# Kernel tuning notes

Hardware: AMD Instinct MI355X
Metric: run time of the kernel (lower is better)

## Reference

```python
import jax, jax.numpy as jnp
import numpy as np


def _silu(v):
    return v * jax.nn.sigmoid(v)


def setup_inputs() -> dict:
    key = jax.random.key(0)
    ks = jax.random.split(key, 12)
    B, N, DS = 4, 12500, 63      # batch, nodes per graph, dim_single
    E = 800000                   # total edges (avg degree 16)
    BN = B * N
    ND = DS + 1                  # node_dim = dim_single + 1 (timestep channel)
    H, ED = 128, 32              # hidden_dim, edge_dim (fixed in __init__)
    MIN = 2 * ND + ED            # m_input feature dim = 160

    def lin(k, i, o):
        return (jax.random.normal(k, (i, o)) / np.sqrt(i)).astype(jnp.float32)

    return {
        "x": jax.random.normal(ks[0], (B, N, 3), dtype=jnp.float32) * 5.0,
        "cond": jax.random.normal(ks[1], (B, N, DS), dtype=jnp.float32),
        "edge_dist": jax.random.uniform(ks[2], (E,), dtype=jnp.float32) * 15.0,
        "ew1": lin(ks[3], 1, ED), "eb1": jnp.zeros((ED,), jnp.float32),
        "ew2": lin(ks[4], ED, ED), "eb2": jnp.zeros((ED,), jnp.float32),
        "nw1": lin(ks[5], MIN, H), "nb1": jnp.zeros((H,), jnp.float32),
        "nw2": lin(ks[6], H, ND), "nb2": jnp.zeros((ND,), jnp.float32),
        "cw1": lin(ks[7], MIN, H), "cb1": jnp.zeros((H,), jnp.float32),
        "cw2": lin(ks[8], H, 1),
        "edge_index": jax.random.randint(ks[9], (2, E), 0, BN, dtype=jnp.int64 if jax.config.jax_enable_x64 else jnp.int32),
        "t": 100,
    }


def reference(x, cond, edge_dist, ew1, eb1, ew2, eb2, nw1, nb1, nw2, nb2,
              cw1, cb1, cw2, edge_index, t):
    B, N, _ = x.shape
    BN = B * N
    # append timestep scalar channel to conditioning -> node features h
    t_feat = jnp.full((B, N, 1), t, dtype=x.dtype)
    h = jnp.concatenate([cond, t_feat], axis=-1).reshape(BN, -1)   # [BN, node_dim]
    xf = x.reshape(BN, 3)

    src, dst = edge_index[0], edge_index[1]
    # edge_mlp on scalar distances -> [E, edge_dim]
    edge_attr = _silu(edge_dist[:, None] @ ew1 + eb1) @ ew2 + eb2
    # gather + concat -> [E, 2*node_dim + edge_dim]
    m_input = jnp.concatenate([h[src], h[dst], edge_attr], axis=-1)
    # node_mlp (its output h_agg is discarded by p_sample, kept for faithfulness)
    m = _silu(m_input @ nw1 + nb1) @ nw2 + nb2
    h_agg = jax.ops.segment_sum(m, dst, num_segments=BN)
    h_out = h + h_agg  # unused by p_sample's return
    del h_out
    # coord_mlp -> scalar weight per edge
    coord_weight = _silu(m_input @ cw1 + cb1) @ cw2                 # [E, 1]
    dir_vec = xf[src] - xf[dst]                                     # [E, 3]
    dir_len = jnp.maximum(jnp.linalg.norm(dir_vec, axis=-1, keepdims=True), 1e-8)
    coord_update = coord_weight * (dir_vec / dir_len)
    x_agg = jax.ops.segment_sum(coord_update, dst, num_segments=BN)
    return (xf + x_agg).reshape(B, N, 3)
```

## Files before the change

### kernel.cpp

```cpp
#include <hip/hip_runtime.h>
#include <hip/hip_bf16.h>

typedef __attribute__((ext_vector_type(8))) short bf16x8;
typedef __attribute__((ext_vector_type(4))) float f32x4;
typedef __attribute__((ext_vector_type(4), aligned(4))) float f32x4u;
typedef __attribute__((ext_vector_type(2), aligned(4))) float f32x2u;

__device__ __forceinline__ unsigned short f2bf(float f) {
    unsigned int u = __float_as_uint(f);
    unsigned int r = (u + 0x7fffu + ((u >> 16) & 1u)) >> 16;
    return (unsigned short)r;
}
__device__ __forceinline__ float bf2f(unsigned short u) {
    return __uint_as_float(((unsigned int)u) << 16);
}

__global__ void init_out_kernel(const float* __restrict__ x, float* __restrict__ out, int n) {
    int i = blockIdx.x * blockDim.x + threadIdx.x;
    if (i < n) out[i] = x[i];
}

__global__ void prep_bt2_kernel(const float* __restrict__ cw1, unsigned short* __restrict__ bt2) {
    int idx = blockIdx.x * 256 + threadIdx.x;
    if (idx < 256 * 64) {
        int n = idx >> 6, k = idx & 63;
        float v = 0.f;
        if (k < 63) v = (n < 128) ? cw1[k * 128 + n] : cw1[(64 + k) * 128 + (n - 128)];
        bt2[n * 64 + k] = f2bf(v);
    }
}

__global__ void prep_consts_kernel(const float* __restrict__ ew2, const float* __restrict__ eb2,
                                   const float* __restrict__ cw1, const float* __restrict__ cb1,
                                   const int* __restrict__ tptr,
                                   unsigned short* __restrict__ bt_M, float* __restrict__ c0) {
    int j = threadIdx.x;
    float t = (float)tptr[0];
    float cacc = cb1[j] + t * (cw1[63 * 128 + j] + cw1[127 * 128 + j]);
    float m[32];
    #pragma unroll
    for (int p = 0; p < 32; ++p) m[p] = 0.f;
    for (int i = 0; i < 32; ++i) {
        float w = cw1[(128 + i) * 128 + j];
        cacc = fmaf(eb2[i], w, cacc);
        #pragma unroll
        for (int p = 0; p < 32; ++p) m[p] = fmaf(ew2[p * 32 + i], w, m[p]);
    }
    c0[j] = cacc;
    #pragma unroll
    for (int p = 0; p < 32; ++p) bt_M[j * 32 + p] = f2bf(m[p]);
}

__device__ __forceinline__ bf16x8 load8_bf(const float* p) {
    f32x4u a = *(const f32x4u*)p;
    f32x4u b = *(const f32x4u*)(p + 4);
    bf16x8 r;
    r[0] = f2bf(a[0]); r[1] = f2bf(a[1]); r[2] = f2bf(a[2]); r[3] = f2bf(a[3]);
    r[4] = f2bf(b[0]); r[5] = f2bf(b[1]); r[6] = f2bf(b[2]); r[7] = f2bf(b[3]);
    return r;
}
__device__ __forceinline__ bf16x8 load7z_bf(const float* p) {
    f32x4u a = *(const f32x4u*)p;
    f32x2u b = *(const f32x2u*)(p + 4);
    float c = p[6];
    bf16x8 r;
    r[0] = f2bf(a[0]); r[1] = f2bf(a[1]); r[2] = f2bf(a[2]); r[3] = f2bf(a[3]);
    r[4] = f2bf(b[0]); r[5] = f2bf(b[1]); r[6] = f2bf(c);  r[7] = 0;
    return r;
}

__global__ __launch_bounds__(256) void prep_uv_kernel(
    const float* __restrict__ cond, const unsigned short* __restrict__ bt2,
    unsigned short* __restrict__ UV, int BN)
{
    const int tid = threadIdx.x, lane = tid & 63, wid = tid >> 6;
    const int fr = lane & 15, kq = lane >> 4;
    int node = blockIdx.x * 64 + wid * 16 + fr;
    if (node >= BN) node = BN - 1;

    const float* cp = cond + (long)node * 63;
    bf16x8 b0 = load8_bf(cp + 8 * kq);
    bf16x8 b1 = (kq < 3) ? load8_bf(cp + 32 + 8 * kq) : load7z_bf(cp + 56);

    char* UVb = (char*)UV;
    const unsigned off = ((unsigned)node * 256u + (unsigned)(kq * 4)) * 2u;

    #pragma unroll
    for (int n = 0; n < 16; ++n) {
        bf16x8 a0 = *reinterpret_cast<const bf16x8*>(&bt2[(n * 16 + fr) * 64 + 8 * kq]);
        bf16x8 a1 = *reinterpret_cast<const bf16x8*>(&bt2[(n * 16 + fr) * 64 + 32 + 8 * kq]);
        f32x4 acc = (f32x4){0.f, 0.f, 0.f, 0.f};
        acc = __builtin_amdgcn_mfma_f32_16x16x32_bf16(a0, b0, acc, 0, 0, 0);
        acc = __builtin_amdgcn_mfma_f32_16x16x32_bf16(a1, b1, acc, 0, 0, 0);
        uint2 pk;
        pk.x = (unsigned)f2bf(acc[0]) | ((unsigned)f2bf(acc[1]) << 16);
        pk.y = (unsigned)f2bf(acc[2]) | ((unsigned)f2bf(acc[3]) << 16);
        *reinterpret_cast<uint2*>(UVb + off + n * 32) = pk;
    }
}

__global__ __launch_bounds__(256, 4) void edge_kernel(
    const float* __restrict__ x, const float* __restrict__ edge_dist,
    const float* __restrict__ ew1, const float* __restrict__ eb1,
    const unsigned short* __restrict__ bt_M, const float* __restrict__ c0f,
    const float* __restrict__ cw2, const unsigned short* __restrict__ UV,
    const int* __restrict__ edge_index, float* __restrict__ out, int E)
{
    __shared__ __align__(16) unsigned short s_lds[128][40];
    __shared__ int srcl[128];
    __shared__ int dstl[128];
    __shared__ float cw_lds[128];

    const int tid = threadIdx.x, lane = tid & 63, wid = tid >> 6;
    const int fr = lane & 15, kq = lane >> 4;
    const int e0 = blockIdx.x * 128;

    {
        int ei = e0 + (tid & 127); if (ei >= E) ei = E - 1;
        if (tid < 128) srcl[tid] = edge_index[ei];
        else           dstl[tid - 128] = edge_index[E + ei];

        int eh = tid >> 1;
        int e  = e0 + eh; if (e >= E) e = E - 1;
        int j0 = (tid & 1) * 16;
        float dist = edge_dist[e];
        #pragma unroll
        for (int i = 0; i < 8; ++i) {
            float v0 = fmaf(dist, ew1[j0 + 2 * i],     eb1[j0 + 2 * i]);
            float v1 = fmaf(dist, ew1[j0 + 2 * i + 1], eb1[j0 + 2 * i + 1]);
            float s0 = v0 / (1.f + __expf(-v0));
            float s1 = v1 / (1.f + __expf(-v1));
            unsigned pk = (unsigned)f2bf(s0) | ((unsigned)f2bf(s1) << 16);
            *reinterpret_cast<unsigned*>(&s_lds[eh][j0 + 2 * i]) = pk;
        }
    }
    __syncthreads();

    bf16x8 a[2];
    #pragma unroll
    for (int m = 0; m < 2; ++m)
        a[m] = *reinterpret_cast<const bf16x8*>(&s_lds[wid * 32 + m * 16 + fr][8 * kq]);

    unsigned bu[2][4], bv[2][4];
    #pragma unroll
    for (int m = 0; m < 2; ++m)
        #pragma unroll
        for (int r = 0; r < 4; ++r) {
            int row = wid * 32 + m * 16 + kq * 4 + r;
            bu[m][r] = ((unsigned)srcl[row] * 256u + (unsigned)fr) * 2u;
            bv[m][r] = ((unsigned)dstl[row] * 256u + 128u + (unsigned)fr) * 2u;
        }

    const char* UVb = (const char*)UV;
    float psum[2][4] = {{0.f,0.f,0.f,0.f},{0.f,0.f,0.f,0.f}};

    #pragma unroll 1
    for (int nh = 0; nh < 2; ++nh) {
        f32x4 acc[2][4];
        #pragma unroll
        for (int n = 0; n < 4; ++n) {
            float c = c0f[(nh * 4 + n) * 16 + fr];
            acc[0][n] = (f32x4){c, c, c, c};
            acc[1][n] = (f32x4){c, c, c, c};
        }
        #pragma unroll
        for (int n = 0; n < 4; ++n) {
            int col = (nh * 4 + n) * 16 + fr;
            bf16x8 b = *reinterpret_cast<const bf16x8*>(&bt_M[col * 32 + 8 * kq]);
            acc[0][n] = __builtin_amdgcn_mfma_f32_16x16x32_bf16(a[0], b, acc[0][n], 0, 0, 0);
            acc[1][n] = __builtin_amdgcn_mfma_f32_16x16x32_bf16(a[1], b, acc[1][n], 0, 0, 0);
        }
        #pragma unroll
        for (int n = 0; n < 4; ++n) {
            float w2 = cw2[(nh * 4 + n) * 16 + fr];
            const int cb = (nh * 4 + n) * 32;
            #pragma unroll
            for (int m = 0; m < 2; ++m)
                #pragma unroll
                for (int r = 0; r < 4; ++r) {
                    unsigned short uu = *reinterpret_cast<const unsigned short*>(UVb + bu[m][r] + cb);
                    unsigned short vv = *reinterpret_cast<const unsigned short*>(UVb + bv[m][r] + cb);
                    float h = acc[m][n][r] + bf2f(uu) + bf2f(vv);
                    float sil = h / (1.f + __expf(-h));
                    psum[m][r] = fmaf(sil, w2, psum[m][r]);
                }
        }
    }

    #pragma unroll
    for (int off = 1; off < 16; off <<= 1)
        #pragma unroll
        for (int m = 0; m < 2; ++m)
            #pragma unroll
            for (int r = 0; r < 4; ++r)
                psum[m][r] += __shfl_xor(psum[m][r], off, 64);
    if (fr == 0) {
        #pragma unroll
        for (int m = 0; m < 2; ++m) {
            int row0 = wid * 32 + m * 16 + kq * 4;
            #pragma unroll
            for (int r = 0; r < 4; ++r) cw_lds[row0 + r] = psum[m][r];
        }
    }
    __syncthreads();

    if (tid < 128) {
        int e = e0 + tid;
        if (e < E) {
            float coord_w = cw_lds[tid];
            int src = srcl[tid];
            int dst = dstl[tid];
            float dx = x[src * 3 + 0] - x[dst * 3 + 0];
            float dy = x[src * 3 + 1] - x[dst * 3 + 1];
            float dz = x[src * 3 + 2] - x[dst * 3 + 2];
            float len = sqrtf(fmaf(dx, dx, fmaf(dy, dy, dz * dz)));
            len = fmaxf(len, 1e-8f);
            float sc = coord_w / len;
            atomicAdd(&out[dst * 3 + 0], sc * dx);
            atomicAdd(&out[dst * 3 + 1], sc * dy);
            atomicAdd(&out[dst * 3 + 2], sc * dz);
        }
    }
}

extern "C" void kernel_launch(void* const* d_in, const int* in_sizes, int n_in,
                              void* d_out, int out_size, void* d_ws, size_t ws_size,
                              hipStream_t stream) {
    const float* x         = (const float*)d_in[0];
    const float* cond      = (const float*)d_in[1];
    const float* edge_dist = (const float*)d_in[2];
    const float* ew1       = (const float*)d_in[3];
    const float* eb1       = (const float*)d_in[4];
    const float* ew2       = (const float*)d_in[5];
    const float* eb2       = (const float*)d_in[6];
    const float* cw1       = (const float*)d_in[11];
    const float* cb1       = (const float*)d_in[12];
    const float* cw2       = (const float*)d_in[13];
    const int*   edge_index= (const int*)d_in[14];
    const int*   tptr      = (const int*)d_in[15];
    float* out = (float*)d_out;

    const int E  = in_sizes[2];
    const int BN = in_sizes[1] / 63;
    const int n_out = out_size;

    char* ws = (char*)d_ws;
    unsigned short* bt_M = (unsigned short*)(ws);
    float*          c0   = (float*)(ws + 8192);
    unsigned short* bt2  = (unsigned short*)(ws + 16384);
    unsigned short* UV   = (unsigned short*)(ws + 65536);

    init_out_kernel<<<(n_out + 255) / 256, 256, 0, stream>>>(x, out, n_out);
    prep_bt2_kernel<<<64, 256, 0, stream>>>(cw1, bt2);
    prep_consts_kernel<<<1, 128, 0, stream>>>(ew2, eb2, cw1, cb1, tptr, bt_M, c0);
    prep_uv_kernel<<<(BN + 63) / 64, 256, 0, stream>>>(cond, bt2, UV, BN);

    int blocks = (E + 127) / 128;
    edge_kernel<<<blocks, 256, 0, stream>>>(x, edge_dist, ew1, eb1,
                                            bt_M, c0, cw2, UV,
                                            edge_index, out, E);
}
```

Baseline: 307.7 us.

## Transpose MFMA operands so each lane gathers contiguous bf16 hidden features per edge

Swaps the MFMA operand roles so the weight matrix is the A operand and edge features the B operand. Each lane then owns one edge and four consecutive hidden columns. The per-node U/V gathers become one 8-byte load of four packed bf16 values instead of four scalar 2-byte loads at scattered rows. The final reduction shrinks from a 4-step 16-lane shuffle tree on eight values to two shuffles on two values. Edge-MLP setup is also reassigned: half the threads compute the edge features and the other half load indices. This may unbalance that setup phase.

```diff
diff --git a/kernel.cpp b/kernel.cpp
--- a/kernel.cpp
+++ b/kernel.cpp
@@ -11,9 +11,8 @@
     unsigned int r = (u + 0x7fffu + ((u >> 16) & 1u)) >> 16;
     return (unsigned short)r;
 }
-__device__ __forceinline__ float bf2f(unsigned short u) {
-    return __uint_as_float(((unsigned int)u) << 16);
-}
+__device__ __forceinline__ float bflo(unsigned int u) { return __uint_as_float(u << 16); }
+__device__ __forceinline__ float bfhi(unsigned int u) { return __uint_as_float(u & 0xffff0000u); }
 
 __global__ void init_out_kernel(const float* __restrict__ x, float* __restrict__ out, int n) {
     int i = blockIdx.x * blockDim.x + threadIdx.x;
@@ -115,92 +114,86 @@
     const int fr = lane & 15, kq = lane >> 4;
     const int e0 = blockIdx.x * 128;
 
-    {
-        int ei = e0 + (tid & 127); if (ei >= E) ei = E - 1;
-        if (tid < 128) srcl[tid] = edge_index[ei];
-        else           dstl[tid - 128] = edge_index[E + ei];
-
-        int eh = tid >> 1;
-        int e  = e0 + eh; if (e >= E) e = E - 1;
-        int j0 = (tid & 1) * 16;
+    if (tid < 128) {
+        int e = e0 + tid; if (e >= E) e = E - 1;
         float dist = edge_dist[e];
         #pragma unroll
-        for (int i = 0; i < 8; ++i) {
-            float v0 = fmaf(dist, ew1[j0 + 2 * i],     eb1[j0 + 2 * i]);
-            float v1 = fmaf(dist, ew1[j0 + 2 * i + 1], eb1[j0 + 2 * i + 1]);
+        for (int i = 0; i < 16; ++i) {
+            float v0 = fmaf(dist, ew1[2 * i],     eb1[2 * i]);
+            float v1 = fmaf(dist, ew1[2 * i + 1], eb1[2 * i + 1]);
             float s0 = v0 / (1.f + __expf(-v0));
             float s1 = v1 / (1.f + __expf(-v1));
             unsigned pk = (unsigned)f2bf(s0) | ((unsigned)f2bf(s1) << 16);
-            *reinterpret_cast<unsigned*>(&s_lds[eh][j0 + 2 * i]) = pk;
-        }
+            *reinterpret_cast<unsigned*>(&s_lds[tid][2 * i]) = pk;
+        }
+    } else {
+        int r = tid - 128;
+        int e = e0 + r; if (e >= E) e = E - 1;
+        srcl[r] = edge_index[e];
+        dstl[r] = edge_index[E + e];
     }
     __syncthreads();
 
-    bf16x8 a[2];
+    bf16x8 sb[2];
     #pragma unroll
     for (int m = 0; m < 2; ++m)
-        a[m] = *reinterpret_cast<const bf16x8*>(&s_lds[wid * 32 + m * 16 + fr][8 * kq]);
-
-    unsigned bu[2][4], bv[2][4];
-    #pragma unroll
-    for (int m = 0; m < 2; ++m)
-        #pragma unroll
-        for (int r = 0; r < 4; ++r) {
-            int row = wid * 32 + m * 16 + kq * 4 + r;
-            bu[m][r] = ((unsigned)srcl[row] * 256u + (unsigned)fr) * 2u;
-            bv[m][r] = ((unsigned)dstl[row] * 256u + 128u + (unsigned)fr) * 2u;
-        }
+        sb[m] = *reinterpret_cast<const bf16x8*>(&s_lds[wid * 32 + m * 16 + fr][8 * kq]);
+
+    unsigned bu[2], bv[2];
+    #pragma unroll
+    for (int m = 0; m < 2; ++m) {
+        int row = wid * 32 + m * 16 + fr;
+        bu[m] = (unsigned)srcl[row] * 512u + (unsigned)(kq * 8);
+        bv[m] = (unsigned)dstl[row] * 512u + 256u + (unsigned)(kq * 8);
+    }
 
     const char* UVb = (const char*)UV;
-    float psum[2][4] = {{0.f,0.f,0.f,0.f},{0.f,0.f,0.f,0.f}};
+    float psum[2] = {0.f, 0.f};
 
     #pragma unroll 1
     for (int nh = 0; nh < 2; ++nh) {
         f32x4 acc[2][4];
         #pragma unroll
         for (int n = 0; n < 4; ++n) {
-            float c = c0f[(nh * 4 + n) * 16 + fr];
-            acc[0][n] = (f32x4){c, c, c, c};
-            acc[1][n] = (f32x4){c, c, c, c};
+            f32x4u c = *reinterpret_cast<const f32x4u*>(c0f + (nh * 4 + n) * 16 + kq * 4);
+            acc[0][n] = (f32x4){c[0], c[1], c[2], c[3]};
+            acc[1][n] = acc[0][n];
         }
         #pragma unroll
         for (int n = 0; n < 4; ++n) {
-            int col = (nh * 4 + n) * 16 + fr;
-            bf16x8 b = *reinterpret_cast<const bf16x8*>(&bt_M[col * 32 + 8 * kq]);
-            acc[0][n] = __builtin_amdgcn_mfma_f32_16x16x32_bf16(a[0], b, acc[0][n], 0, 0, 0);
-            acc[1][n] = __builtin_amdgcn_mfma_f32_16x16x32_bf16(a[1], b, acc[1][n], 0, 0, 0);
+            bf16x8 aw = *reinterpret_cast<const bf16x8*>(&bt_M[((nh * 4 + n) * 16 + fr) * 32 + 8 * kq]);
+            acc[0][n] = __builtin_amdgcn_mfma_f32_16x16x32_bf16(aw, sb[0], acc[0][n], 0, 0, 0);
+            acc[1][n] = __builtin_amdgcn_mfma_f32_16x16x32_bf16(aw, sb[1], acc[1][n], 0, 0, 0);
         }
         #pragma unroll
         for (int n = 0; n < 4; ++n) {
-            float w2 = cw2[(nh * 4 + n) * 16 + fr];
+            f32x4u w2 = *reinterpret_cast<const f32x4u*>(cw2 + (nh * 4 + n) * 16 + kq * 4);
             const int cb = (nh * 4 + n) * 32;
             #pragma unroll
-            for (int m = 0; m < 2; ++m)
+            for (int m = 0; m < 2; ++m) {
+                uint2 uu = *reinterpret_cast<const uint2*>(UVb + bu[m] + cb);
+                uint2 vv = *reinterpret_cast<const uint2*>(UVb + bv[m] + cb);
+                float uf[4] = {bflo(uu.x), bfhi(uu.x), bflo(uu.y), bfhi(uu.y)};
+                float vf[4] = {bflo(vv.x), bfhi(vv.x), bflo(vv.y), bfhi(vv.y)};
                 #pragma unroll
                 for (int r = 0; r < 4; ++r) {
-                    unsigned short uu = *reinterpret_cast<const unsigned short*>(UVb + bu[m][r] + cb);
-                    unsigned short vv = *reinterpret_cast<const unsigned short*>(UVb + bv[m][r] + cb);
-                    float h = acc[m][n][r] + bf2f(uu) + bf2f(vv);
+                    float h = acc[m][n][r] + uf[r] + vf[r];
                     float sil = h / (1.f + __expf(-h));
-                    psum[m][r] = fmaf(sil, w2, psum[m][r]);
+                    psum[m] = fmaf(sil, w2[r], psum[m]);
                 }
-        }
-    }
-
-    #pragma unroll
-    for (int off = 1; off < 16; off <<= 1)
+            }
+        }
+    }
+
+    #pragma unroll
+    for (int m = 0; m < 2; ++m) {
+        psum[m] += __shfl_xor(psum[m], 16, 64);
+        psum[m] += __shfl_xor(psum[m], 32, 64);
+    }
+    if (kq == 0) {
         #pragma unroll
         for (int m = 0; m < 2; ++m)
-            #pragma unroll
-            for (int r = 0; r < 4; ++r)
-                psum[m][r] += __shfl_xor(psum[m][r], off, 64);
-    if (fr == 0) {
-        #pragma unroll
-        for (int m = 0; m < 2; ++m) {
-            int row0 = wid * 32 + m * 16 + kq * 4;
-            #pragma unroll
-            for (int r = 0; r < 4; ++r) cw_lds[row0 + r] = psum[m][r];
-        }
+            cw_lds[wid * 32 + m * 16 + fr] = psum[m];
     }
     __syncthreads();
 
```

After: 286.7 us. -6.8%, faster.
